# Kernel optimization log

Measured on AMD Instinct MI355X. Metric: run time of the kernel, lower is better.

Reference implementation:

```python
import jax, jax.numpy as jnp
import numpy as np

SMOOTH = 4.0      # smoothness_factor
MAX_RATE = 2.0    # maximum_rate
MIN_RATE = 0.0    # minimum_rate
MIN_SHAPE = 1.0   # minimum_shape per dim
INIT_RATE = 1.0   # initial rates value -> determines static output shape


def dct_mat(N):
    """Orthonormal DCT-II matrix: (dct_mat(N) @ x) == dct(x, norm='ortho').

    Mathematically identical to the FFT-based butterfly in the torch source
    with norm='ortho'.
    """
    n = np.arange(N)[None, :]
    k = np.arange(N)[:, None]
    D = np.cos(np.pi * (2 * n + 1) * k / (2 * N)) * np.sqrt(2.0 / N)
    D[0] *= 1.0 / np.sqrt(2.0)
    return jnp.asarray(D, dtype=jnp.float32)


def span_mask(threshold, softness, pos):
    # adaptive-span ramp mask (Sukhbaatar et al. 2019), clamped to [0, 1]
    return jnp.clip((softness + threshold - pos) / softness, 0.0, 1.0)


def setup_inputs() -> dict:
    key = jax.random.key(0)
    x = jax.random.normal(key, (32, 64, 128, 128), dtype=jnp.float32)
    rate_weights = jnp.ones((2,), dtype=jnp.float32)  # nn.Parameter init = rates
    return {"x": x, "rate_weights": rate_weights}


def reference(x, rate_weights):
    B, C, H, W = x.shape
    cur = jnp.array([H, W], dtype=jnp.float32)

    # rate clamping (maximum_shape is None -> constrain_max_shape stays False)
    min_allowed = jnp.maximum((jnp.array([MIN_SHAPE, MIN_SHAPE]) - SMOOTH) / cur,
                              jnp.array([MIN_RATE, MIN_RATE]))
    max_allowed = jnp.array([MAX_RATE, MAX_RATE], dtype=jnp.float32)
    r = jnp.clip(rate_weights, min_allowed, max_allowed)

    new_smooth = cur * r + SMOOTH  # traced float, drives the soft mask
    # static output shape from the initial rate values (jit-compatible;
    # matches torch's int(new_shape_smooth) + 1 for the init rates)
    new_h = int(H * INIT_RATE + SMOOTH) + 1  # H + 5
    new_w = int(W * INIT_RATE + SMOOTH) + 1  # W + 5

    # 2D orthonormal DCT-II over the last two dims
    Dh, Dw = dct_mat(H), dct_mat(W)
    freq = jnp.einsum('ui,bcij,vj->bcuv', Dh, x, Dw)  # [B,C,H,W]

    # zero-pad high frequencies up to the new (larger) shape
    freq = jnp.pad(freq, ((0, 0), (0, 0),
                          (0, max(new_h - H, 0)), (0, max(new_w - W, 0))))

    # adaptive-span masks over frequency positions
    vpos = jnp.arange(new_h, dtype=jnp.float32)
    hpos = jnp.arange(new_w, dtype=jnp.float32)
    crop = new_smooth - SMOOTH  # = cur * r
    vmask = span_mask(crop[0], SMOOTH, vpos)  # [new_h]
    hmask = span_mask(crop[1], SMOOTH, hpos)  # [new_w]
    freq = freq * vmask[None, None, :, None] * hmask[None, None, None, :]

    # 2D orthonormal inverse DCT (DCT-III) at the new resolution
    Dh2, Dw2 = dct_mat(new_h), dct_mat(new_w)
    out = jnp.einsum('ui,bcuv,vj->bcij', Dh2, freq, Dw2)  # [B,C,new_h,new_w]
    return out
```

## Files before the change

### kernel.cpp

```cpp
#include <hip/hip_runtime.h>
#include <hip/hip_bf16.h>
#include <math.h>

#define NSLICE 2048
#define NH 133
#define NP 144
#define NT 576

#define M1B  32768
#define SCR  69632
#define LDSB 78848

typedef __attribute__((ext_vector_type(8))) short bf16x8;
typedef __attribute__((ext_vector_type(4))) float f32x4;

typedef __attribute__((address_space(3))) unsigned int  lds_u32;
typedef const __attribute__((address_space(1))) unsigned int glb_u32;

#define GLOAD_LDS16(gsrc, ldst) \
    __builtin_amdgcn_global_load_lds((glb_u32*)(gsrc), (lds_u32*)(ldst), 16, 0, 0)

__device__ __forceinline__ unsigned f2bf(float f) {
    __hip_bfloat16 h = __float2bfloat16(f);
    union { __hip_bfloat16 b; unsigned short u; } c; c.b = h; return (unsigned)c.u;
}

__global__ void prep_M(const float* __restrict__ rw,
                       unsigned short* __restrict__ M1,
                       unsigned short* __restrict__ M2) {
    __shared__ float t1[512];
    __shared__ float t2[532];
    const int b   = blockIdx.x;
    const int m   = b / NP;
    const int row = b - m * NP;
    const int p   = threadIdx.x;

    const float c1  = (float)(M_PI / 256.0);
    const float c2  = (float)(M_PI / 266.0);
    const float s1n = 0.125f;
    const float s10 = 0.08838834764831844f;
    const float s2n = 0.12262786485246718f;
    const float s20 = 0.08671099951921386f;

    for (int k = p; k < 512; k += 128) t1[k] = cosf((float)k * c1) * s1n;
    for (int k = p; k < 532; k += 128) t2[k] = cosf((float)k * c2) * s2n;
    __syncthreads();

    float val = 0.0f;
    if (row < NH) {
        float r = rw[m];
        float minr = fmaxf((1.0f - 4.0f) / 128.0f, 0.0f);
        r = fminf(fmaxf(r, minr), 2.0f);
        const float crop = 128.0f * r;

        const int tp = 2 * p + 1;
        const int ti = 2 * row + 1;
        float acc = s10 * s20;
        int a1 = 0, a2 = 0;
        for (int u = 1; u < 128; ++u) {
            a1 = (a1 + tp) & 511;
            a2 += ti; if (a2 >= 532) a2 -= 532;
            float mask = fminf(fmaxf((4.0f + crop - (float)u) * 0.25f, 0.0f), 1.0f);
            acc = fmaf(t1[a1] * mask, t2[a2], acc);
        }
        val = acc;
    }
    const unsigned short v16 = (unsigned short)f2bf(val);
    if (m == 0) {
        const int it = row >> 4, rr = row & 15;
        const int k2 = p >> 5, gg = (p >> 3) & 3, e = p & 7;
        M1[(size_t)((it * 4 + k2) * 512 + (gg * 16 + rr) * 8 + e)] = v16;
    } else {
        M2[(size_t)row * 128 + p] = v16;
    }
}

__global__ __launch_bounds__(NT, 5) void dct_resize(
        const float* __restrict__ x,
        const unsigned short* __restrict__ M1f,
        const unsigned short* __restrict__ M2,
        float* __restrict__ out) {
    __shared__ __align__(16) unsigned char lds[LDSB];

    const int tid  = threadIdx.x;
    const int w    = tid >> 6;
    const int lane = tid & 63;
    const int r    = lane & 15;
    const int g    = lane >> 4;

    const float* xs = x + (size_t)blockIdx.x * (128 * 128);
    float*       os = out + (size_t)blockIdx.x * (NH * NH);

    const int j0 = w * 16;

    #pragma unroll
    for (int v = 0; v < 4; ++v)
        GLOAD_LDS16(M1f + (size_t)(v * NT + tid) * 8,
                    lds + M1B + (v * NT + tid) * 16);

    bf16x8 bm2[4];
    #pragma unroll
    for (int kk = 0; kk < 4; ++kk)
        bm2[kk] = *(const bf16x8*)(M2 + (size_t)(j0 + r) * 128 + kk * 32 + g * 8);

    if (w < 8) {
        #pragma unroll
        for (int v = 0; v < 4; ++v) {
            const int f  = v * 8 + w;
            const int pt = f >> 2, k2 = f & 3;
            const float* src = xs + (size_t)(pt * 16 + r) * 128 + k2 * 32 + g * 8;
            const float4 lo = *(const float4*)src;
            const float4 hi = *(const float4*)(src + 4);
            uint4 pkt;
            pkt.x = f2bf(lo.x) | (f2bf(lo.y) << 16);
            pkt.y = f2bf(lo.z) | (f2bf(lo.w) << 16);
            pkt.z = f2bf(hi.x) | (f2bf(hi.y) << 16);
            pkt.w = f2bf(hi.z) | (f2bf(hi.w) << 16);
            *(uint4*)(lds + f * 1024 + lane * 16) = pkt;
        }
    }
    __syncthreads();

    uint2 u2[8];
    #pragma unroll
    for (int pt = 0; pt < 8; ++pt) {
        f32x4 acc = {0.f, 0.f, 0.f, 0.f};
        #pragma unroll
        for (int kk = 0; kk < 4; ++kk) {
            bf16x8 a = *(const bf16x8*)(lds + (pt * 4 + kk) * 1024 + lane * 16);
            acc = __builtin_amdgcn_mfma_f32_16x16x32_bf16(a, bm2[kk], acc, 0, 0, 0);
        }
        u2[pt].x = f2bf(acc[0]) | (f2bf(acc[1]) << 16);
        u2[pt].y = f2bf(acc[2]) | (f2bf(acc[3]) << 16);
    }

    unsigned char* scr = lds + SCR + w * 1024;
    bf16x8 bfrag[4];
    #pragma unroll
    for (int kk = 0; kk < 4; ++kk) {
        *(uint2*)(scr + (g)     * 128 + r * 8) = u2[2 * kk];
        *(uint2*)(scr + (4 + g) * 128 + r * 8) = u2[2 * kk + 1];
        const uint2 lo2 = *(const uint2*)(scr + (2 * g)     * 128 + r * 8);
        const uint2 hi2 = *(const uint2*)(scr + (2 * g + 1) * 128 + r * 8);
        union { uint4 u; bf16x8 b; } cv;
        cv.u = make_uint4(lo2.x, lo2.y, hi2.x, hi2.y);
        bfrag[kk] = cv.b;
    }

    const int jc = j0 + r;
    #pragma unroll
    for (int it = 0; it < 9; ++it) {
        f32x4 acc = {0.f, 0.f, 0.f, 0.f};
        #pragma unroll
        for (int kk = 0; kk < 4; ++kk) {
            bf16x8 a = *(const bf16x8*)(lds + M1B + (it * 4 + kk) * 1024 + lane * 16);
            acc = __builtin_amdgcn_mfma_f32_16x16x32_bf16(a, bfrag[kk], acc, 0, 0, 0);
        }
        if (jc < NH) {
            #pragma unroll
            for (int q = 0; q < 4; ++q) {
                const int i = it * 16 + g * 4 + q;
                if (i < NH) os[(size_t)i * NH + jc] = acc[q];
            }
        }
    }
}

extern "C" void kernel_launch(void* const* d_in, const int* in_sizes, int n_in,
                              void* d_out, int out_size, void* d_ws, size_t ws_size,
                              hipStream_t stream) {
    const float* x  = (const float*)d_in[0];
    const float* rw = (const float*)d_in[1];
    float* outp = (float*)d_out;
    unsigned short* M1 = (unsigned short*)d_ws;
    unsigned short* M2 = M1 + 18432;

    prep_M<<<dim3(2 * NP), dim3(128), 0, stream>>>(rw, M1, M2);
    dct_resize<<<dim3(NSLICE), dim3(NT), 0, stream>>>(x, M1, M2, outp);
}
```

Before: 76.32 us.

## Process four slices per block with async global-to-LDS pipelined strip loads

Each block now handles four slices instead of one and streams fp32 input strips straight into LDS through global_load_lds, keeping three strips in flight in a four-deep ring buffer with swizzled layout. The fp32-to-bf16 conversion moves to the point where fragments are read from LDS. The M1 and M2 matrix loads are now spread over four slices per block, and input loads overlap compute. The trade-offs are fewer blocks (512), a barrier per strip, and a lower occupancy hint.

```diff
diff --git a/kernel.cpp b/kernel.cpp
--- a/kernel.cpp
+++ b/kernel.cpp
@@ -6,6 +6,9 @@
 #define NH 133
 #define NP 144
 #define NT 576
+#define SPB 4
+#define NBLK (NSLICE / SPB)
+#define NSTRIP (SPB * 8)
 
 #define M1B  32768
 #define SCR  69632
@@ -19,6 +22,12 @@
 
 #define GLOAD_LDS16(gsrc, ldst) \
     __builtin_amdgcn_global_load_lds((glb_u32*)(gsrc), (lds_u32*)(ldst), 16, 0, 0)
+
+#define VMW(n)  asm volatile("s_waitcnt vmcnt(" #n ")" ::: "memory")
+#define BAR() do { __builtin_amdgcn_sched_barrier(0); \
+                   asm volatile("s_waitcnt lgkmcnt(0)" ::: "memory"); \
+                   __builtin_amdgcn_s_barrier(); \
+                   __builtin_amdgcn_sched_barrier(0); } while (0)
 
 __device__ __forceinline__ unsigned f2bf(float f) {
     __hip_bfloat16 h = __float2bfloat16(f);
@@ -75,7 +84,7 @@
     }
 }
 
-__global__ __launch_bounds__(NT, 5) void dct_resize(
+__global__ __launch_bounds__(NT, 4) void dct_resize(
         const float* __restrict__ x,
         const unsigned short* __restrict__ M1f,
         const unsigned short* __restrict__ M2,
@@ -88,82 +97,97 @@
     const int r    = lane & 15;
     const int g    = lane >> 4;
 
-    const float* xs = x + (size_t)blockIdx.x * (128 * 128);
-    float*       os = out + (size_t)blockIdx.x * (NH * NH);
+    const float* xbase = x   + (size_t)blockIdx.x * SPB * (128 * 128);
+    float*       obase = out + (size_t)blockIdx.x * SPB * (NH * NH);
 
     const int j0 = w * 16;
+
+    bf16x8 bm2[4];
+    #pragma unroll
+    for (int kk = 0; kk < 4; ++kk)
+        bm2[kk] = *(const bf16x8*)(M2 + (size_t)(j0 + r) * 128 + kk * 32 + g * 8);
+    VMW(0);
+    __builtin_amdgcn_sched_barrier(0);
+
+    const int srow = (tid >> 5) & 15;
+    const int sgc  = (tid & 31) ^ (srow & 7);
+
+    #define ISSUE(n) do { if (tid < 512 && (n) < NSTRIP) {                     \
+        const float* _s = xbase + (size_t)((n) >> 3) * (128 * 128)             \
+                        + (size_t)((((n) & 7) * 16 + srow) * 128) + sgc * 4;   \
+        GLOAD_LDS16(_s, lds + ((n) & 3) * 8192 + tid * 16); } } while (0)
 
     #pragma unroll
     for (int v = 0; v < 4; ++v)
         GLOAD_LDS16(M1f + (size_t)(v * NT + tid) * 8,
                     lds + M1B + (v * NT + tid) * 16);
-
-    bf16x8 bm2[4];
+    ISSUE(0); ISSUE(1); ISSUE(2);
+
     #pragma unroll
-    for (int kk = 0; kk < 4; ++kk)
-        bm2[kk] = *(const bf16x8*)(M2 + (size_t)(j0 + r) * 128 + kk * 32 + g * 8);
-
-    if (w < 8) {
+    for (int s = 0; s < SPB; ++s) {
+        uint2 u2[8];
         #pragma unroll
-        for (int v = 0; v < 4; ++v) {
-            const int f  = v * 8 + w;
-            const int pt = f >> 2, k2 = f & 3;
-            const float* src = xs + (size_t)(pt * 16 + r) * 128 + k2 * 32 + g * 8;
-            const float4 lo = *(const float4*)src;
-            const float4 hi = *(const float4*)(src + 4);
-            uint4 pkt;
-            pkt.x = f2bf(lo.x) | (f2bf(lo.y) << 16);
-            pkt.y = f2bf(lo.z) | (f2bf(lo.w) << 16);
-            pkt.z = f2bf(hi.x) | (f2bf(hi.y) << 16);
-            pkt.w = f2bf(hi.z) | (f2bf(hi.w) << 16);
-            *(uint4*)(lds + f * 1024 + lane * 16) = pkt;
-        }
-    }
-    __syncthreads();
-
-    uint2 u2[8];
-    #pragma unroll
-    for (int pt = 0; pt < 8; ++pt) {
-        f32x4 acc = {0.f, 0.f, 0.f, 0.f};
+        for (int p8 = 0; p8 < 8; ++p8) {
+            const int n = s * 8 + p8;
+            if (s == 0 || p8 >= 3) { VMW(2); } else { VMW(38); }
+            BAR();
+            ISSUE(n + 3);
+
+            const unsigned char* sb = lds + (n & 3) * 8192 + r * 512;
+            f32x4 acc = {0.f, 0.f, 0.f, 0.f};
+            #pragma unroll
+            for (int kk = 0; kk < 4; ++kk) {
+                const int c0 = kk * 8 + g * 2;
+                const float4 lo = *(const float4*)(sb + ((c0)     ^ (r & 7)) * 16);
+                const float4 hi = *(const float4*)(sb + ((c0 + 1) ^ (r & 7)) * 16);
+                union { bf16x8 b; unsigned short us[8]; } fr;
+                fr.us[0] = (unsigned short)f2bf(lo.x);
+                fr.us[1] = (unsigned short)f2bf(lo.y);
+                fr.us[2] = (unsigned short)f2bf(lo.z);
+                fr.us[3] = (unsigned short)f2bf(lo.w);
+                fr.us[4] = (unsigned short)f2bf(hi.x);
+                fr.us[5] = (unsigned short)f2bf(hi.y);
+                fr.us[6] = (unsigned short)f2bf(hi.z);
+                fr.us[7] = (unsigned short)f2bf(hi.w);
+                acc = __builtin_amdgcn_mfma_f32_16x16x32_bf16(fr.b, bm2[kk], acc, 0, 0, 0);
+            }
+            u2[p8].x = f2bf(acc[0]) | (f2bf(acc[1]) << 16);
+            u2[p8].y = f2bf(acc[2]) | (f2bf(acc[3]) << 16);
+        }
+
+        unsigned char* scr = lds + SCR + w * 1024;
+        bf16x8 bfrag[4];
         #pragma unroll
         for (int kk = 0; kk < 4; ++kk) {
-            bf16x8 a = *(const bf16x8*)(lds + (pt * 4 + kk) * 1024 + lane * 16);
-            acc = __builtin_amdgcn_mfma_f32_16x16x32_bf16(a, bm2[kk], acc, 0, 0, 0);
-        }
-        u2[pt].x = f2bf(acc[0]) | (f2bf(acc[1]) << 16);
-        u2[pt].y = f2bf(acc[2]) | (f2bf(acc[3]) << 16);
+            *(uint2*)(scr + (g)     * 128 + r * 8) = u2[2 * kk];
+            *(uint2*)(scr + (4 + g) * 128 + r * 8) = u2[2 * kk + 1];
+            const uint2 lo2 = *(const uint2*)(scr + (2 * g)     * 128 + r * 8);
+            const uint2 hi2 = *(const uint2*)(scr + (2 * g + 1) * 128 + r * 8);
+            union { uint4 u; bf16x8 b; } cv;
+            cv.u = make_uint4(lo2.x, lo2.y, hi2.x, hi2.y);
+            bfrag[kk] = cv.b;
+        }
+
+        float* os = obase + (size_t)s * (NH * NH);
+        const int jc = j0 + r;
+        #pragma unroll
+        for (int it = 0; it < 9; ++it) {
+            f32x4 acc = {0.f, 0.f, 0.f, 0.f};
+            #pragma unroll
+            for (int kk = 0; kk < 4; ++kk) {
+                bf16x8 a = *(const bf16x8*)(lds + M1B + (it * 4 + kk) * 1024 + lane * 16);
+                acc = __builtin_amdgcn_mfma_f32_16x16x32_bf16(a, bfrag[kk], acc, 0, 0, 0);
+            }
+            if (jc < NH) {
+                #pragma unroll
+                for (int q = 0; q < 4; ++q) {
+                    const int i = it * 16 + g * 4 + q;
+                    if (i < NH) os[(size_t)i * NH + jc] = acc[q];
+                }
+            }
+        }
     }
-
-    unsigned char* scr = lds + SCR + w * 1024;
-    bf16x8 bfrag[4];
-    #pragma unroll
-    for (int kk = 0; kk < 4; ++kk) {
-        *(uint2*)(scr + (g)     * 128 + r * 8) = u2[2 * kk];
-        *(uint2*)(scr + (4 + g) * 128 + r * 8) = u2[2 * kk + 1];
-        const uint2 lo2 = *(const uint2*)(scr + (2 * g)     * 128 + r * 8);
-        const uint2 hi2 = *(const uint2*)(scr + (2 * g + 1) * 128 + r * 8);
-        union { uint4 u; bf16x8 b; } cv;
-        cv.u = make_uint4(lo2.x, lo2.y, hi2.x, hi2.y);
-        bfrag[kk] = cv.b;
-    }
-
-    const int jc = j0 + r;
-    #pragma unroll
-    for (int it = 0; it < 9; ++it) {
-        f32x4 acc = {0.f, 0.f, 0.f, 0.f};
-        #pragma unroll
-        for (int kk = 0; kk < 4; ++kk) {
-            bf16x8 a = *(const bf16x8*)(lds + M1B + (it * 4 + kk) * 1024 + lane * 16);
-            acc = __builtin_amdgcn_mfma_f32_16x16x32_bf16(a, bfrag[kk], acc, 0, 0, 0);
-        }
-        if (jc < NH) {
-            #pragma unroll
-            for (int q = 0; q < 4; ++q) {
-                const int i = it * 16 + g * 4 + q;
-                if (i < NH) os[(size_t)i * NH + jc] = acc[q];
-            }
-        }
-    }
+    #undef ISSUE
 }
 
 extern "C" void kernel_launch(void* const* d_in, const int* in_sizes, int n_in,
@@ -176,5 +200,5 @@
     unsigned short* M2 = M1 + 18432;
 
     prep_M<<<dim3(2 * NP), dim3(128), 0, stream>>>(rw, M1, M2);
-    dct_resize<<<dim3(NSLICE), dim3(NT), 0, stream>>>(x, M1, M2, outp);
-}
+    dct_resize<<<dim3(NBLK), dim3(NT), 0, stream>>>(x, M1, M2, outp);
+}
```

Result: slower. 102.5 us (+34.3%).

## Process eight slices per block with async prefetch of next slice into LDS

Applied to the files above, without the earlier changes.

Each block now handles eight slices instead of one, cutting the grid to 256 blocks. M1 is loaded once per block and amortised across the slices. The next slice's raw fp32 data is streamed into LDS via global_load_lds while the current slice runs its MFMAs. In exchange, LDS use grows to about 141 KB per block, which caps occupancy at one or two blocks per CU, and 256 blocks may underfill the 256 CUs' worth of latency hiding.

```diff
diff --git a/kernel.cpp b/kernel.cpp
--- a/kernel.cpp
+++ b/kernel.cpp
@@ -6,10 +6,13 @@
 #define NH 133
 #define NP 144
 #define NT 576
-
-#define M1B  32768
-#define SCR  69632
-#define LDSB 78848
+#define SPB 8
+#define NBLK (NSLICE / SPB)
+
+#define XFM  65536
+#define M1B  98304
+#define SCR  135168
+#define LDSB 144384
 
 typedef __attribute__((ext_vector_type(8))) short bf16x8;
 typedef __attribute__((ext_vector_type(4))) float f32x4;
@@ -75,7 +78,7 @@
     }
 }
 
-__global__ __launch_bounds__(NT, 5) void dct_resize(
+__global__ __launch_bounds__(NT, 2) void dct_resize(
         const float* __restrict__ x,
         const unsigned short* __restrict__ M1f,
         const unsigned short* __restrict__ M2,
@@ -88,82 +91,103 @@
     const int r    = lane & 15;
     const int g    = lane >> 4;
 
-    const float* xs = x + (size_t)blockIdx.x * (128 * 128);
-    float*       os = out + (size_t)blockIdx.x * (NH * NH);
+    const float* xbase = x   + (size_t)blockIdx.x * SPB * (128 * 128);
+    float*       obase = out + (size_t)blockIdx.x * SPB * (NH * NH);
 
     const int j0 = w * 16;
+
+    #define ISSUE_X(sl) do { if (w < 8) {                                      \
+        const float* _xs = xbase + (size_t)(sl) * (128 * 128);                 \
+        _Pragma("unroll")                                                      \
+        for (int v = 0; v < 8; ++v) {                                          \
+            const int hf = w * 8 + v;                                          \
+            const int f_ = hf >> 1, h_ = hf & 1;                               \
+            const int pt_ = f_ >> 2, k2_ = f_ & 3;                             \
+            const float* _src = _xs + (size_t)(pt_ * 16 + r) * 128             \
+                              + k2_ * 32 + g * 8 + h_ * 4;                     \
+            GLOAD_LDS16(_src, lds + hf * 1024);           \
+        } } } while (0)
 
     #pragma unroll
     for (int v = 0; v < 4; ++v)
         GLOAD_LDS16(M1f + (size_t)(v * NT + tid) * 8,
                     lds + M1B + (v * NT + tid) * 16);
+    ISSUE_X(0);
 
     bf16x8 bm2[4];
     #pragma unroll
     for (int kk = 0; kk < 4; ++kk)
         bm2[kk] = *(const bf16x8*)(M2 + (size_t)(j0 + r) * 128 + kk * 32 + g * 8);
 
-    if (w < 8) {
+    __syncthreads();
+
+    for (int s = 0; s < SPB; ++s) {
+        if (w < 8) {
+            #pragma unroll
+            for (int v = 0; v < 4; ++v) {
+                const int f = v * 8 + w;
+                const float4 lo = *(const float4*)(lds + (2 * f) * 1024 + lane * 16);
+                const float4 hi = *(const float4*)(lds + (2 * f + 1) * 1024 + lane * 16);
+                uint4 pkt;
+                pkt.x = f2bf(lo.x) | (f2bf(lo.y) << 16);
+                pkt.y = f2bf(lo.z) | (f2bf(lo.w) << 16);
+                pkt.z = f2bf(hi.x) | (f2bf(hi.y) << 16);
+                pkt.w = f2bf(hi.z) | (f2bf(hi.w) << 16);
+                *(uint4*)(lds + XFM + f * 1024 + lane * 16) = pkt;
+            }
+        }
+        __syncthreads();
+
+        if (s + 1 < SPB) ISSUE_X(s + 1);
+
+        uint2 u2[8];
         #pragma unroll
-        for (int v = 0; v < 4; ++v) {
-            const int f  = v * 8 + w;
-            const int pt = f >> 2, k2 = f & 3;
-            const float* src = xs + (size_t)(pt * 16 + r) * 128 + k2 * 32 + g * 8;
-            const float4 lo = *(const float4*)src;
-            const float4 hi = *(const float4*)(src + 4);
-            uint4 pkt;
-            pkt.x = f2bf(lo.x) | (f2bf(lo.y) << 16);
-            pkt.y = f2bf(lo.z) | (f2bf(lo.w) << 16);
-            pkt.z = f2bf(hi.x) | (f2bf(hi.y) << 16);
-            pkt.w = f2bf(hi.z) | (f2bf(hi.w) << 16);
-            *(uint4*)(lds + f * 1024 + lane * 16) = pkt;
-        }
-    }
-    __syncthreads();
-
-    uint2 u2[8];
-    #pragma unroll
-    for (int pt = 0; pt < 8; ++pt) {
-        f32x4 acc = {0.f, 0.f, 0.f, 0.f};
+        for (int pt = 0; pt < 8; ++pt) {
+            f32x4 acc = {0.f, 0.f, 0.f, 0.f};
+            #pragma unroll
+            for (int kk = 0; kk < 4; ++kk) {
+                bf16x8 a = *(const bf16x8*)(lds + XFM + (pt * 4 + kk) * 1024 + lane * 16);
+                acc = __builtin_amdgcn_mfma_f32_16x16x32_bf16(a, bm2[kk], acc, 0, 0, 0);
+            }
+            u2[pt].x = f2bf(acc[0]) | (f2bf(acc[1]) << 16);
+            u2[pt].y = f2bf(acc[2]) | (f2bf(acc[3]) << 16);
+        }
+
+        unsigned char* scr = lds + SCR + w * 1024;
+        bf16x8 bfrag[4];
         #pragma unroll
         for (int kk = 0; kk < 4; ++kk) {
-            bf16x8 a = *(const bf16x8*)(lds + (pt * 4 + kk) * 1024 + lane * 16);
-            acc = __builtin_amdgcn_mfma_f32_16x16x32_bf16(a, bm2[kk], acc, 0, 0, 0);
-        }
-        u2[pt].x = f2bf(acc[0]) | (f2bf(acc[1]) << 16);
-        u2[pt].y = f2bf(acc[2]) | (f2bf(acc[3]) << 16);
+            *(uint2*)(scr + (g)     * 128 + r * 8) = u2[2 * kk];
+            *(uint2*)(scr + (4 + g) * 128 + r * 8) = u2[2 * kk + 1];
+            const uint2 lo2 = *(const uint2*)(scr + (2 * g)     * 128 + r * 8);
+            const uint2 hi2 = *(const uint2*)(scr + (2 * g + 1) * 128 + r * 8);
+            union { uint4 u; bf16x8 b; } cv;
+            cv.u = make_uint4(lo2.x, lo2.y, hi2.x, hi2.y);
+            bfrag[kk] = cv.b;
+        }
+
+        float* os = obase + (size_t)s * (NH * NH);
+        const int jc = j0 + r;
+        #pragma unroll
+        for (int it = 0; it < 9; ++it) {
+            f32x4 acc = {0.f, 0.f, 0.f, 0.f};
+            #pragma unroll
+            for (int kk = 0; kk < 4; ++kk) {
+                bf16x8 a = *(const bf16x8*)(lds + M1B + (it * 4 + kk) * 1024 + lane * 16);
+                acc = __builtin_amdgcn_mfma_f32_16x16x32_bf16(a, bfrag[kk], acc, 0, 0, 0);
+            }
+            if (jc < NH) {
+                #pragma unroll
+                for (int q = 0; q < 4; ++q) {
+                    const int i = it * 16 + g * 4 + q;
+                    if (i < NH) os[(size_t)i * NH + jc] = acc[q];
+                }
+            }
+        }
+
+        __syncthreads();
     }
-
-    unsigned char* scr = lds + SCR + w * 1024;
-    bf16x8 bfrag[4];
-    #pragma unroll
-    for (int kk = 0; kk < 4; ++kk) {
-        *(uint2*)(scr + (g)     * 128 + r * 8) = u2[2 * kk];
-        *(uint2*)(scr + (4 + g) * 128 + r * 8) = u2[2 * kk + 1];
-        const uint2 lo2 = *(const uint2*)(scr + (2 * g)     * 128 + r * 8);
-        const uint2 hi2 = *(const uint2*)(scr + (2 * g + 1) * 128 + r * 8);
-        union { uint4 u; bf16x8 b; } cv;
-        cv.u = make_uint4(lo2.x, lo2.y, hi2.x, hi2.y);
-        bfrag[kk] = cv.b;
-    }
-
-    const int jc = j0 + r;
-    #pragma unroll
-    for (int it = 0; it < 9; ++it) {
-        f32x4 acc = {0.f, 0.f, 0.f, 0.f};
-        #pragma unroll
-        for (int kk = 0; kk < 4; ++kk) {
-            bf16x8 a = *(const bf16x8*)(lds + M1B + (it * 4 + kk) * 1024 + lane * 16);
-            acc = __builtin_amdgcn_mfma_f32_16x16x32_bf16(a, bfrag[kk], acc, 0, 0, 0);
-        }
-        if (jc < NH) {
-            #pragma unroll
-            for (int q = 0; q < 4; ++q) {
-                const int i = it * 16 + g * 4 + q;
-                if (i < NH) os[(size_t)i * NH + jc] = acc[q];
-            }
-        }
-    }
+    #undef ISSUE_X
 }
 
 extern "C" void kernel_launch(void* const* d_in, const int* in_sizes, int n_in,
@@ -176,5 +200,5 @@
     unsigned short* M2 = M1 + 18432;
 
     prep_M<<<dim3(2 * NP), dim3(128), 0, stream>>>(rw, M1, M2);
-    dct_resize<<<dim3(NSLICE), dim3(NT), 0, stream>>>(x, M1, M2, outp);
-}
+    dct_resize<<<dim3(NBLK), dim3(NT), 0, stream>>>(x, M1, M2, outp);
+}
```

Measured after the change: 72.17 us. 5.4% less time.

## Process four slices per block with double-buffered async global-to-LDS x loads

Applied to the files above, without the earlier changes.

Each block now handles four slices instead of one. The M1/M2 matrix load cost is paid once per block rather than once per slice. Input x is streamed in strips through double-buffered LDS using global_load_lds, with explicit waitcnt and barriers, so the next strip loads while the current one is converted to bf16 and multiplied. This cuts the grid to 512 blocks and lowers occupancy to 4, which risks poorer load balance across CUs and adds extra barrier overhead per strip.

```diff
diff --git a/kernel.cpp b/kernel.cpp
--- a/kernel.cpp
+++ b/kernel.cpp
@@ -6,6 +6,9 @@
 #define NH 133
 #define NP 144
 #define NT 576
+#define SPB 4
+#define NBLK (NSLICE / SPB)
+#define NSTRIPS (SPB * 4)
 
 #define M1B  32768
 #define SCR  69632
@@ -19,6 +22,13 @@
 
 #define GLOAD_LDS16(gsrc, ldst) \
     __builtin_amdgcn_global_load_lds((glb_u32*)(gsrc), (lds_u32*)(ldst), 16, 0, 0)
+
+#define VMW0  asm volatile("s_waitcnt vmcnt(0)" ::: "memory")
+#define VMW36 asm volatile("s_waitcnt vmcnt(36)" ::: "memory")
+#define BAR() do { __builtin_amdgcn_sched_barrier(0); \
+                   asm volatile("s_waitcnt lgkmcnt(0)" ::: "memory"); \
+                   __builtin_amdgcn_s_barrier(); \
+                   __builtin_amdgcn_sched_barrier(0); } while (0)
 
 __device__ __forceinline__ unsigned f2bf(float f) {
     __hip_bfloat16 h = __float2bfloat16(f);
@@ -75,7 +85,7 @@
     }
 }
 
-__global__ __launch_bounds__(NT, 5) void dct_resize(
+__global__ __launch_bounds__(NT, 4) void dct_resize(
         const float* __restrict__ x,
         const unsigned short* __restrict__ M1f,
         const unsigned short* __restrict__ M2,
@@ -88,82 +98,104 @@
     const int r    = lane & 15;
     const int g    = lane >> 4;
 
-    const float* xs = x + (size_t)blockIdx.x * (128 * 128);
-    float*       os = out + (size_t)blockIdx.x * (NH * NH);
+    const float* xbase = x   + (size_t)blockIdx.x * SPB * (128 * 128);
+    float*       obase = out + (size_t)blockIdx.x * SPB * (NH * NH);
 
     const int j0 = w * 16;
+
+    #define ISSUE_STRIP(n_) do { if (w < 8 && (n_) < NSTRIPS) {                \
+        const float* _xs = xbase + (size_t)((n_) >> 2) * (128 * 128);          \
+        const int pt_ = 2 * ((n_) & 3) + (w >> 2);                             \
+        const float* s0 = _xs + (size_t)(pt_ * 16 + r) * 128                   \
+                        + (w & 3) * 32 + g * 8;                                \
+        GLOAD_LDS16(s0,     lds + ((n_) & 1) * 16384 + (2 * w) * 1024);        \
+        GLOAD_LDS16(s0 + 4, lds + ((n_) & 1) * 16384 + (2 * w + 1) * 1024);    \
+    } } while (0)
+
+    bf16x8 bm2[4];
+    #pragma unroll
+    for (int kk = 0; kk < 4; ++kk)
+        bm2[kk] = *(const bf16x8*)(M2 + (size_t)(j0 + r) * 128 + kk * 32 + g * 8);
+    asm volatile("" :: "v"(bm2[0]), "v"(bm2[1]), "v"(bm2[2]), "v"(bm2[3]));
+    VMW0;
+    __builtin_amdgcn_sched_barrier(0);
 
     #pragma unroll
     for (int v = 0; v < 4; ++v)
         GLOAD_LDS16(M1f + (size_t)(v * NT + tid) * 8,
                     lds + M1B + (v * NT + tid) * 16);
-
-    bf16x8 bm2[4];
-    #pragma unroll
-    for (int kk = 0; kk < 4; ++kk)
-        bm2[kk] = *(const bf16x8*)(M2 + (size_t)(j0 + r) * 128 + kk * 32 + g * 8);
-
-    if (w < 8) {
+    ISSUE_STRIP(0);
+    __syncthreads();
+
+    for (int s = 0; s < SPB; ++s) {
+        uint2 u2[8];
         #pragma unroll
-        for (int v = 0; v < 4; ++v) {
-            const int f  = v * 8 + w;
-            const int pt = f >> 2, k2 = f & 3;
-            const float* src = xs + (size_t)(pt * 16 + r) * 128 + k2 * 32 + g * 8;
-            const float4 lo = *(const float4*)src;
-            const float4 hi = *(const float4*)(src + 4);
-            uint4 pkt;
-            pkt.x = f2bf(lo.x) | (f2bf(lo.y) << 16);
-            pkt.y = f2bf(lo.z) | (f2bf(lo.w) << 16);
-            pkt.z = f2bf(hi.x) | (f2bf(hi.y) << 16);
-            pkt.w = f2bf(hi.z) | (f2bf(hi.w) << 16);
-            *(uint4*)(lds + f * 1024 + lane * 16) = pkt;
-        }
-    }
-    __syncthreads();
-
-    uint2 u2[8];
-    #pragma unroll
-    for (int pt = 0; pt < 8; ++pt) {
-        f32x4 acc = {0.f, 0.f, 0.f, 0.f};
+        for (int t = 0; t < 4; ++t) {
+            const int n = s * 4 + t;
+            if (t == 0) { VMW36; } else { VMW0; }
+            BAR();
+            ISSUE_STRIP(n + 1);
+
+            unsigned char* B = lds + (n & 1) * 16384;
+            if (w < 8) {
+                const float4 lo = *(const float4*)(B + (2 * w) * 1024 + lane * 16);
+                const float4 hi = *(const float4*)(B + (2 * w + 1) * 1024 + lane * 16);
+                uint4 pkt;
+                pkt.x = f2bf(lo.x) | (f2bf(lo.y) << 16);
+                pkt.y = f2bf(lo.z) | (f2bf(lo.w) << 16);
+                pkt.z = f2bf(hi.x) | (f2bf(hi.y) << 16);
+                pkt.w = f2bf(hi.z) | (f2bf(hi.w) << 16);
+                *(uint4*)(B + w * 2048 + lane * 16) = pkt;
+            }
+            BAR();
+
+            #pragma unroll
+            for (int d = 0; d < 2; ++d) {
+                f32x4 acc = {0.f, 0.f, 0.f, 0.f};
+                #pragma unroll
+                for (int kk = 0; kk < 4; ++kk) {
+                    bf16x8 a = *(const bf16x8*)(B + (d * 4 + kk) * 2048 + lane * 16);
+                    acc = __builtin_amdgcn_mfma_f32_16x16x32_bf16(a, bm2[kk], acc, 0, 0, 0);
+                }
+                const int pt = 2 * t + d;
+                u2[pt].x = f2bf(acc[0]) | (f2bf(acc[1]) << 16);
+                u2[pt].y = f2bf(acc[2]) | (f2bf(acc[3]) << 16);
+            }
+        }
+
+        unsigned char* scr = lds + SCR + w * 1024;
+        bf16x8 bfrag[4];
         #pragma unroll
         for (int kk = 0; kk < 4; ++kk) {
-            bf16x8 a = *(const bf16x8*)(lds + (pt * 4 + kk) * 1024 + lane * 16);
-            acc = __builtin_amdgcn_mfma_f32_16x16x32_bf16(a, bm2[kk], acc, 0, 0, 0);
-        }
-        u2[pt].x = f2bf(acc[0]) | (f2bf(acc[1]) << 16);
-        u2[pt].y = f2bf(acc[2]) | (f2bf(acc[3]) << 16);
+            *(uint2*)(scr + (g)     * 128 + r * 8) = u2[2 * kk];
+            *(uint2*)(scr + (4 + g) * 128 + r * 8) = u2[2 * kk + 1];
+            const uint2 lo2 = *(const uint2*)(scr + (2 * g)     * 128 + r * 8);
+            const uint2 hi2 = *(const uint2*)(scr + (2 * g + 1) * 128 + r * 8);
+            union { uint4 u; bf16x8 b; } cv;
+            cv.u = make_uint4(lo2.x, lo2.y, hi2.x, hi2.y);
+            bfrag[kk] = cv.b;
+        }
+
+        float* os = obase + (size_t)s * (NH * NH);
+        const int jc = j0 + r;
+        #pragma unroll
+        for (int it = 0; it < 9; ++it) {
+            f32x4 acc = {0.f, 0.f, 0.f, 0.f};
+            #pragma unroll
+            for (int kk = 0; kk < 4; ++kk) {
+                bf16x8 a = *(const bf16x8*)(lds + M1B + (it * 4 + kk) * 1024 + lane * 16);
+                acc = __builtin_amdgcn_mfma_f32_16x16x32_bf16(a, bfrag[kk], acc, 0, 0, 0);
+            }
+            if (jc < NH) {
+                #pragma unroll
+                for (int q = 0; q < 4; ++q) {
+                    const int i = it * 16 + g * 4 + q;
+                    if (i < NH) os[(size_t)i * NH + jc] = acc[q];
+                }
+            }
+        }
     }
-
-    unsigned char* scr = lds + SCR + w * 1024;
-    bf16x8 bfrag[4];
-    #pragma unroll
-    for (int kk = 0; kk < 4; ++kk) {
-        *(uint2*)(scr + (g)     * 128 + r * 8) = u2[2 * kk];
-        *(uint2*)(scr + (4 + g) * 128 + r * 8) = u2[2 * kk + 1];
-        const uint2 lo2 = *(const uint2*)(scr + (2 * g)     * 128 + r * 8);
-        const uint2 hi2 = *(const uint2*)(scr + (2 * g + 1) * 128 + r * 8);
-        union { uint4 u; bf16x8 b; } cv;
-        cv.u = make_uint4(lo2.x, lo2.y, hi2.x, hi2.y);
-        bfrag[kk] = cv.b;
-    }
-
-    const int jc = j0 + r;
-    #pragma unroll
-    for (int it = 0; it < 9; ++it) {
-        f32x4 acc = {0.f, 0.f, 0.f, 0.f};
-        #pragma unroll
-        for (int kk = 0; kk < 4; ++kk) {
-            bf16x8 a = *(const bf16x8*)(lds + M1B + (it * 4 + kk) * 1024 + lane * 16);
-            acc = __builtin_amdgcn_mfma_f32_16x16x32_bf16(a, bfrag[kk], acc, 0, 0, 0);
-        }
-        if (jc < NH) {
-            #pragma unroll
-            for (int q = 0; q < 4; ++q) {
-                const int i = it * 16 + g * 4 + q;
-                if (i < NH) os[(size_t)i * NH + jc] = acc[q];
-            }
-        }
-    }
+    #undef ISSUE_STRIP
 }
 
 extern "C" void kernel_launch(void* const* d_in, const int* in_sizes, int n_in,
@@ -176,5 +208,5 @@
     unsigned short* M2 = M1 + 18432;
 
     prep_M<<<dim3(2 * NP), dim3(128), 0, stream>>>(rw, M1, M2);
-    dct_resize<<<dim3(NSLICE), dim3(NT), 0, stream>>>(x, M1, M2, outp);
-}
+    dct_resize<<<dim3(NBLK), dim3(NT), 0, stream>>>(x, M1, M2, outp);
+}
```

Measured after the change: 89.85 us. +17.7%, slower.
